# Kernel optimization log

Hardware: AMD Instinct MI355X
Metric: run time of the kernel (lower is better)

Reference implementation:

```python
import jax, jax.numpy as jnp
import numpy as np


def setup_inputs() -> dict:
    key = jax.random.key(0)
    ks = jax.random.split(key, 7)
    B, N, H, BIN = 16, 96, 256, 11
    std = 0.1
    return {
        "inputs": jax.random.normal(ks[0], (B, N, H), dtype=jnp.float32),
        "bin_features": jax.random.normal(ks[1], (B, N, N, BIN), dtype=jnp.float32),
        "W_atom": jax.random.normal(ks[2], (H, H), dtype=jnp.float32) * std,
        "W_bin": jax.random.normal(ks[3], (BIN, H), dtype=jnp.float32) * std,
        "b_bin": jnp.zeros((H,), dtype=jnp.float32),
        "w_score": jax.random.normal(ks[4], (H, 1), dtype=jnp.float32) * std,
        "b_score": jnp.zeros((1,), dtype=jnp.float32),
    }


def reference(inputs, bin_features, W_atom, W_bin, b_bin, w_score, b_score):
    # inputs: [B, N, H]; bin_features: [B, N, N, BIN]
    h1 = inputs[:, None, :, :]            # [B, 1, N, H] (atom_hiddens1)
    h2 = inputs[:, :, None, :]            # [B, N, 1, H] (atom_hiddens2)
    atom_pair = h1 + h2                   # [B, N, N, H]
    # Dense(no bias) on pair + Dense(bias) on bin features, then relu
    att_hidden = jax.nn.relu(
        jnp.einsum("bijh,hk->bijk", atom_pair, W_atom)
        + jnp.einsum("bijc,ck->bijk", bin_features, W_bin)
        + b_bin
    )                                      # [B, N, N, H]
    att_score = jax.nn.sigmoid(jnp.einsum("bijk,ko->bijo", att_hidden, w_score) + b_score)  # [B, N, N, 1]
    # att_context = score * atom_hiddens1 (broadcast over i), summed over j (axis 2)
    context = jnp.einsum("bijo,bjh->bih", att_score, inputs)  # [B, N, H]
    return context, atom_pair
```

## Files before the change

kernel.cpp:

```cpp
#include <hip/hip_runtime.h>
#include <math.h>

#define BB 16
#define NN 96
#define HH 256
#define NBIN 11
#define NBPAD 12

template <int CTRL>
__device__ __forceinline__ float dpp_add(float x) {
    int t = __builtin_amdgcn_update_dpp(0, __float_as_int(x),
                                        CTRL, 0xf, 0xf, true);
    return x + __int_as_float(t);
}

__device__ __forceinline__ float wave64_sum_uniform(float x) {
    x = dpp_add<0x111>(x);
    x = dpp_add<0x112>(x);
    x = dpp_add<0x114>(x);
    x = dpp_add<0x118>(x);
    x = dpp_add<0x142>(x);
    x = dpp_add<0x143>(x);
    return __int_as_float(__builtin_amdgcn_readlane(__float_as_int(x), 63));
}

#define ROWS_PER_BLOCK 4

__global__ __launch_bounds__(HH) void proj_kernel(
    const float* __restrict__ inputs,
    const float* __restrict__ W_atom,
    const float* __restrict__ b_bin,
    float* __restrict__ proj)
{
    __shared__ float rows[ROWS_PER_BLOCK][HH];
    const int r0 = blockIdx.x * ROWS_PER_BLOCK;
    const int k  = threadIdx.x;

    #pragma unroll
    for (int r = 0; r < ROWS_PER_BLOCK; ++r)
        rows[r][k] = inputs[(size_t)(r0 + r) * HH + k];
    __syncthreads();

    float acc[ROWS_PER_BLOCK];
    #pragma unroll
    for (int r = 0; r < ROWS_PER_BLOCK; ++r) acc[r] = 0.f;

    #pragma unroll 8
    for (int h = 0; h < HH; ++h) {
        const float w = W_atom[(size_t)h * HH + k];
        #pragma unroll
        for (int r = 0; r < ROWS_PER_BLOCK; ++r)
            acc[r] = fmaf(rows[r][h], w, acc[r]);
    }

    const float halfb = 0.5f * b_bin[k];
    #pragma unroll
    for (int r = 0; r < ROWS_PER_BLOCK; ++r)
        proj[(size_t)(r0 + r) * HH + k] = acc[r] + halfb;
}

__global__ __launch_bounds__(256) void pair_ctx_kernel(
    const float* __restrict__ inputs,
    const float* __restrict__ bin_features,
    const float* __restrict__ W_bin,
    const float* __restrict__ w_score,
    const float* __restrict__ b_score,
    const float* __restrict__ proj,
    float* __restrict__ atom_pair,
    float* __restrict__ context)
{
    const int bi   = blockIdx.x;
    const int b    = bi / NN;
    const int lane = threadIdx.x & 63;
    const int wave = threadIdx.x >> 6;
    const int k4   = lane << 2;

    __shared__ float binf[NN * NBPAD];
    __shared__ float partial[3][HH];

    {
        const float* bp = bin_features + (size_t)bi * NN * NBIN;
        for (int t = threadIdx.x; t < NN * NBIN; t += 256)
            binf[(t / NBIN) * NBPAD + (t % NBIN)] = bp[t];
    }

    const float4 in_i = *(const float4*)(inputs + (size_t)bi * HH + k4);
    const float4 pr_i = *(const float4*)(proj   + (size_t)bi * HH + k4);
    const float4 ws   = *(const float4*)(w_score + k4);
    const float  bsc  = b_score[0];

    float4 wb[NBIN];
    #pragma unroll
    for (int c = 0; c < NBIN; ++c)
        wb[c] = *(const float4*)(W_bin + c * HH + k4);

    const float* inb = inputs + (size_t)b * NN * HH + k4;
    const float* prb = proj   + (size_t)b * NN * HH + k4;
    float*       apb = atom_pair + (size_t)bi * NN * HH + k4;

    __syncthreads();

    float4 acc = make_float4(0.f, 0.f, 0.f, 0.f);

    for (int t = 0; t < 6; ++t) {
        const int j0 = wave + 16 * t;

        float4 inj[4], prj[4];
        #pragma unroll
        for (int u = 0; u < 4; ++u) {
            inj[u] = *(const float4*)(inb + (size_t)(j0 + 4 * u) * HH);
            prj[u] = *(const float4*)(prb + (size_t)(j0 + 4 * u) * HH);
        }

        #pragma unroll
        for (int u = 0; u < 4; ++u) {
            float4 ap;
            ap.x = in_i.x + inj[u].x;  ap.y = in_i.y + inj[u].y;
            ap.z = in_i.z + inj[u].z;  ap.w = in_i.w + inj[u].w;
            *(float4*)(apb + (size_t)(j0 + 4 * u) * HH) = ap;
        }

        float part[4];
        #pragma unroll
        for (int u = 0; u < 4; ++u) {
            const float4* bf4 = (const float4*)&binf[(j0 + 4 * u) * NBPAD];
            const float4 bq0 = bf4[0];
            const float4 bq1 = bf4[1];
            const float4 bq2 = bf4[2];
            const float bc[NBIN] = { bq0.x, bq0.y, bq0.z, bq0.w,
                                     bq1.x, bq1.y, bq1.z, bq1.w,
                                     bq2.x, bq2.y, bq2.z };

            float4 v;
            v.x = pr_i.x + prj[u].x;  v.y = pr_i.y + prj[u].y;
            v.z = pr_i.z + prj[u].z;  v.w = pr_i.w + prj[u].w;
            #pragma unroll
            for (int c = 0; c < NBIN; ++c) {
                v.x = fmaf(bc[c], wb[c].x, v.x);
                v.y = fmaf(bc[c], wb[c].y, v.y);
                v.z = fmaf(bc[c], wb[c].z, v.z);
                v.w = fmaf(bc[c], wb[c].w, v.w);
            }
            v.x = fmaxf(v.x, 0.f); v.y = fmaxf(v.y, 0.f);
            v.z = fmaxf(v.z, 0.f); v.w = fmaxf(v.w, 0.f);
            part[u] = v.x * ws.x + v.y * ws.y + v.z * ws.z + v.w * ws.w;
        }

        float s[4];
        #pragma unroll
        for (int u = 0; u < 4; ++u) {
            const float tot = wave64_sum_uniform(part[u]);
            s[u] = 1.f / (1.f + __expf(-(tot + bsc)));
        }

        #pragma unroll
        for (int u = 0; u < 4; ++u) {
            acc.x = fmaf(s[u], inj[u].x, acc.x);
            acc.y = fmaf(s[u], inj[u].y, acc.y);
            acc.z = fmaf(s[u], inj[u].z, acc.z);
            acc.w = fmaf(s[u], inj[u].w, acc.w);
        }
    }

    if (wave > 0) *(float4*)(&partial[wave - 1][k4]) = acc;
    __syncthreads();
    if (wave == 0) {
        #pragma unroll
        for (int w = 0; w < 3; ++w) {
            const float4 pw = *(const float4*)(&partial[w][k4]);
            acc.x += pw.x; acc.y += pw.y; acc.z += pw.z; acc.w += pw.w;
        }
        *(float4*)(context + (size_t)bi * HH + k4) = acc;
    }
}

extern "C" void kernel_launch(void* const* d_in, const int* in_sizes, int n_in,
                              void* d_out, int out_size, void* d_ws, size_t ws_size,
                              hipStream_t stream)
{
    const float* inputs       = (const float*)d_in[0];
    const float* bin_features = (const float*)d_in[1];
    const float* W_atom       = (const float*)d_in[2];
    const float* W_bin        = (const float*)d_in[3];
    const float* b_bin        = (const float*)d_in[4];
    const float* w_score      = (const float*)d_in[5];
    const float* b_score      = (const float*)d_in[6];

    float* context   = (float*)d_out;
    float* atom_pair = (float*)d_out + (size_t)BB * NN * HH;

    float* proj = (float*)d_ws;

    proj_kernel<<<(BB * NN) / ROWS_PER_BLOCK, HH, 0, stream>>>(
        inputs, W_atom, b_bin, proj);

    pair_ctx_kernel<<<BB * NN, 256, 0, stream>>>(
        inputs, bin_features, W_bin, w_score, b_score, proj,
        atom_pair, context);
}
```

Measured before the change: 51.72 us.

## Warp-specialize pair kernel: two waves store atom_pair, two compute scores

Splits the four waves of each block by role. Waves 2-3 only read inputs rows and stream the large atom_pair output, while waves 0-1 do the bin-feature projection, ReLU, score reduction and context accumulation over all 96 j. The aim is to overlap the store-bound atom_pair traffic with the compute-bound score path and to shrink the shared-memory partial reduction. The risk is that the compute waves now each handle twice as many j values, so the critical path may lengthen. The two roles also rely on matching __syncthreads counts across divergent branches.

```diff
diff --git a/kernel.cpp b/kernel.cpp
--- a/kernel.cpp
+++ b/kernel.cpp
@@ -76,7 +76,7 @@
     const int k4   = lane << 2;
 
     __shared__ float binf[NN * NBPAD];
-    __shared__ float partial[3][HH];
+    __shared__ float partial[HH];
 
     {
         const float* bp = bin_features + (size_t)bi * NN * NBIN;
@@ -84,93 +84,106 @@
             binf[(t / NBIN) * NBPAD + (t % NBIN)] = bp[t];
     }
 
-    const float4 in_i = *(const float4*)(inputs + (size_t)bi * HH + k4);
-    const float4 pr_i = *(const float4*)(proj   + (size_t)bi * HH + k4);
-    const float4 ws   = *(const float4*)(w_score + k4);
-    const float  bsc  = b_score[0];
-
-    float4 wb[NBIN];
-    #pragma unroll
-    for (int c = 0; c < NBIN; ++c)
-        wb[c] = *(const float4*)(W_bin + c * HH + k4);
-
     const float* inb = inputs + (size_t)b * NN * HH + k4;
-    const float* prb = proj   + (size_t)b * NN * HH + k4;
-    float*       apb = atom_pair + (size_t)bi * NN * HH + k4;
-
-    __syncthreads();
-
-    float4 acc = make_float4(0.f, 0.f, 0.f, 0.f);
-
-    for (int t = 0; t < 6; ++t) {
-        const int j0 = wave + 16 * t;
-
-        float4 inj[4], prj[4];
+
+    if (wave >= 2) {
+        const float4 in_i = *(const float4*)(inputs + (size_t)bi * HH + k4);
+        float* apb = atom_pair + (size_t)bi * NN * HH + k4;
+        const int ww = wave - 2;
+
+        __syncthreads();
+
+        for (int t = 0; t < 12; ++t) {
+            const int j0 = 8 * t + 4 * ww;
+            float4 r[4];
+            #pragma unroll
+            for (int u = 0; u < 4; ++u)
+                r[u] = *(const float4*)(inb + (size_t)(j0 + u) * HH);
+            #pragma unroll
+            for (int u = 0; u < 4; ++u) {
+                float4 ap;
+                ap.x = in_i.x + r[u].x;  ap.y = in_i.y + r[u].y;
+                ap.z = in_i.z + r[u].z;  ap.w = in_i.w + r[u].w;
+                *(float4*)(apb + (size_t)(j0 + u) * HH) = ap;
+            }
+        }
+
+        __syncthreads();
+    } else {
+        const float4 pr_i = *(const float4*)(proj + (size_t)bi * HH + k4);
+        const float4 ws   = *(const float4*)(w_score + k4);
+        const float  bsc  = b_score[0];
+
+        float4 wb[NBIN];
         #pragma unroll
-        for (int u = 0; u < 4; ++u) {
-            inj[u] = *(const float4*)(inb + (size_t)(j0 + 4 * u) * HH);
-            prj[u] = *(const float4*)(prb + (size_t)(j0 + 4 * u) * HH);
+        for (int c = 0; c < NBIN; ++c)
+            wb[c] = *(const float4*)(W_bin + c * HH + k4);
+
+        const float* prb = proj + (size_t)b * NN * HH + k4;
+
+        __syncthreads();
+
+        float4 acc = make_float4(0.f, 0.f, 0.f, 0.f);
+
+        for (int t = 0; t < 12; ++t) {
+            const int j0 = 8 * t + 4 * wave;
+
+            float4 inj[4], prj[4];
+            #pragma unroll
+            for (int u = 0; u < 4; ++u) {
+                inj[u] = *(const float4*)(inb + (size_t)(j0 + u) * HH);
+                prj[u] = *(const float4*)(prb + (size_t)(j0 + u) * HH);
+            }
+
+            float part[4];
+            #pragma unroll
+            for (int u = 0; u < 4; ++u) {
+                const float4* bf4 = (const float4*)&binf[(j0 + u) * NBPAD];
+                const float4 bq0 = bf4[0];
+                const float4 bq1 = bf4[1];
+                const float4 bq2 = bf4[2];
+                const float bc[NBIN] = { bq0.x, bq0.y, bq0.z, bq0.w,
+                                         bq1.x, bq1.y, bq1.z, bq1.w,
+                                         bq2.x, bq2.y, bq2.z };
+
+                float4 v;
+                v.x = pr_i.x + prj[u].x;  v.y = pr_i.y + prj[u].y;
+                v.z = pr_i.z + prj[u].z;  v.w = pr_i.w + prj[u].w;
+                #pragma unroll
+                for (int c = 0; c < NBIN; ++c) {
+                    v.x = fmaf(bc[c], wb[c].x, v.x);
+                    v.y = fmaf(bc[c], wb[c].y, v.y);
+                    v.z = fmaf(bc[c], wb[c].z, v.z);
+                    v.w = fmaf(bc[c], wb[c].w, v.w);
+                }
+                v.x = fmaxf(v.x, 0.f); v.y = fmaxf(v.y, 0.f);
+                v.z = fmaxf(v.z, 0.f); v.w = fmaxf(v.w, 0.f);
+                part[u] = v.x * ws.x + v.y * ws.y + v.z * ws.z + v.w * ws.w;
+            }
+
+            float s[4];
+            #pragma unroll
+            for (int u = 0; u < 4; ++u) {
+                const float tot = wave64_sum_uniform(part[u]);
+                s[u] = 1.f / (1.f + __expf(-(tot + bsc)));
+            }
+
+            #pragma unroll
+            for (int u = 0; u < 4; ++u) {
+                acc.x = fmaf(s[u], inj[u].x, acc.x);
+                acc.y = fmaf(s[u], inj[u].y, acc.y);
+                acc.z = fmaf(s[u], inj[u].z, acc.z);
+                acc.w = fmaf(s[u], inj[u].w, acc.w);
+            }
         }
 
-        #pragma unroll
-        for (int u = 0; u < 4; ++u) {
-            float4 ap;
-            ap.x = in_i.x + inj[u].x;  ap.y = in_i.y + inj[u].y;
-            ap.z = in_i.z + inj[u].z;  ap.w = in_i.w + inj[u].w;
-            *(float4*)(apb + (size_t)(j0 + 4 * u) * HH) = ap;
+        if (wave == 1) *(float4*)(&partial[k4]) = acc;
+        __syncthreads();
+        if (wave == 0) {
+            const float4 pw = *(const float4*)(&partial[k4]);
+            acc.x += pw.x; acc.y += pw.y; acc.z += pw.z; acc.w += pw.w;
+            *(float4*)(context + (size_t)bi * HH + k4) = acc;
         }
-
-        float part[4];
-        #pragma unroll
-        for (int u = 0; u < 4; ++u) {
-            const float4* bf4 = (const float4*)&binf[(j0 + 4 * u) * NBPAD];
-            const float4 bq0 = bf4[0];
-            const float4 bq1 = bf4[1];
-            const float4 bq2 = bf4[2];
-            const float bc[NBIN] = { bq0.x, bq0.y, bq0.z, bq0.w,
-                                     bq1.x, bq1.y, bq1.z, bq1.w,
-                                     bq2.x, bq2.y, bq2.z };
-
-            float4 v;
-            v.x = pr_i.x + prj[u].x;  v.y = pr_i.y + prj[u].y;
-            v.z = pr_i.z + prj[u].z;  v.w = pr_i.w + prj[u].w;
-            #pragma unroll
-            for (int c = 0; c < NBIN; ++c) {
-                v.x = fmaf(bc[c], wb[c].x, v.x);
-                v.y = fmaf(bc[c], wb[c].y, v.y);
-                v.z = fmaf(bc[c], wb[c].z, v.z);
-                v.w = fmaf(bc[c], wb[c].w, v.w);
-            }
-            v.x = fmaxf(v.x, 0.f); v.y = fmaxf(v.y, 0.f);
-            v.z = fmaxf(v.z, 0.f); v.w = fmaxf(v.w, 0.f);
-            part[u] = v.x * ws.x + v.y * ws.y + v.z * ws.z + v.w * ws.w;
-        }
-
-        float s[4];
-        #pragma unroll
-        for (int u = 0; u < 4; ++u) {
-            const float tot = wave64_sum_uniform(part[u]);
-            s[u] = 1.f / (1.f + __expf(-(tot + bsc)));
-        }
-
-        #pragma unroll
-        for (int u = 0; u < 4; ++u) {
-            acc.x = fmaf(s[u], inj[u].x, acc.x);
-            acc.y = fmaf(s[u], inj[u].y, acc.y);
-            acc.z = fmaf(s[u], inj[u].z, acc.z);
-            acc.w = fmaf(s[u], inj[u].w, acc.w);
-        }
-    }
-
-    if (wave > 0) *(float4*)(&partial[wave - 1][k4]) = acc;
-    __syncthreads();
-    if (wave == 0) {
-        #pragma unroll
-        for (int w = 0; w < 3; ++w) {
-            const float4 pw = *(const float4*)(&partial[w][k4]);
-            acc.x += pw.x; acc.y += pw.y; acc.z += pw.z; acc.w += pw.w;
-        }
-        *(float4*)(context + (size_t)bi * HH + k4) = acc;
     }
 }
 
```

New measurement: 65.12 us. +25.9%, slower.

## Process two query rows per block to reuse j-row loads across i

Applied to the files above, without the earlier changes.

The pair/context kernel now handles two consecutive i rows per block, so each loaded inputs[j] and proj[j] float4 serves both rows. This halves the global reads of j-side data and halves the grid size. Launch bounds now request 4 blocks per CU, and the projection kernel uses 3 rows per block, giving more blocks there. The risks are higher register pressure from the two accumulators and fewer blocks to spread across the CUs.

```diff
diff --git a/kernel.cpp b/kernel.cpp
--- a/kernel.cpp
+++ b/kernel.cpp
@@ -6,6 +6,7 @@
 #define HH 256
 #define NBIN 11
 #define NBPAD 12
+#define IB 2
 
 template <int CTRL>
 __device__ __forceinline__ float dpp_add(float x) {
@@ -24,7 +25,7 @@
     return __int_as_float(__builtin_amdgcn_readlane(__float_as_int(x), 63));
 }
 
-#define ROWS_PER_BLOCK 4
+#define ROWS_PER_BLOCK 3
 
 __global__ __launch_bounds__(HH) void proj_kernel(
     const float* __restrict__ inputs,
@@ -59,7 +60,7 @@
         proj[(size_t)(r0 + r) * HH + k] = acc[r] + halfb;
 }
 
-__global__ __launch_bounds__(256) void pair_ctx_kernel(
+__global__ __launch_bounds__(256, 4) void pair_ctx_kernel(
     const float* __restrict__ inputs,
     const float* __restrict__ bin_features,
     const float* __restrict__ W_bin,
@@ -69,108 +70,134 @@
     float* __restrict__ atom_pair,
     float* __restrict__ context)
 {
-    const int bi   = blockIdx.x;
-    const int b    = bi / NN;
+    const int blk  = blockIdx.x;
+    const int b    = blk / (NN / IB);
+    const int ip   = blk % (NN / IB);
+    const int bi0  = b * NN + IB * ip;
     const int lane = threadIdx.x & 63;
     const int wave = threadIdx.x >> 6;
     const int k4   = lane << 2;
 
-    __shared__ float binf[NN * NBPAD];
-    __shared__ float partial[3][HH];
+    __shared__ float binf[IB * NN * NBPAD];
+    __shared__ float partial[3][IB * HH];
 
     {
-        const float* bp = bin_features + (size_t)bi * NN * NBIN;
-        for (int t = threadIdx.x; t < NN * NBIN; t += 256)
+        const float* bp = bin_features + (size_t)bi0 * NN * NBIN;
+        for (int t = threadIdx.x; t < IB * NN * NBIN; t += 256)
             binf[(t / NBIN) * NBPAD + (t % NBIN)] = bp[t];
     }
 
-    const float4 in_i = *(const float4*)(inputs + (size_t)bi * HH + k4);
-    const float4 pr_i = *(const float4*)(proj   + (size_t)bi * HH + k4);
-    const float4 ws   = *(const float4*)(w_score + k4);
-    const float  bsc  = b_score[0];
+    const float4 in_i0 = *(const float4*)(inputs + (size_t)bi0 * HH + k4);
+    const float4 in_i1 = *(const float4*)(inputs + (size_t)(bi0 + 1) * HH + k4);
+    const float4 pr_i0 = *(const float4*)(proj   + (size_t)bi0 * HH + k4);
+    const float4 pr_i1 = *(const float4*)(proj   + (size_t)(bi0 + 1) * HH + k4);
+    const float4 ws    = *(const float4*)(w_score + k4);
+    const float  bsc   = b_score[0];
 
     float4 wb[NBIN];
     #pragma unroll
     for (int c = 0; c < NBIN; ++c)
         wb[c] = *(const float4*)(W_bin + c * HH + k4);
 
-    const float* inb = inputs + (size_t)b * NN * HH + k4;
-    const float* prb = proj   + (size_t)b * NN * HH + k4;
-    float*       apb = atom_pair + (size_t)bi * NN * HH + k4;
+    const float* inb  = inputs + (size_t)b * NN * HH + k4;
+    const float* prb  = proj   + (size_t)b * NN * HH + k4;
+    float*       apb0 = atom_pair + (size_t)bi0 * NN * HH + k4;
+    float*       apb1 = atom_pair + (size_t)(bi0 + 1) * NN * HH + k4;
 
     __syncthreads();
 
-    float4 acc = make_float4(0.f, 0.f, 0.f, 0.f);
-
-    for (int t = 0; t < 6; ++t) {
-        const int j0 = wave + 16 * t;
-
-        float4 inj[4], prj[4];
-        #pragma unroll
-        for (int u = 0; u < 4; ++u) {
+    float4 acc0 = make_float4(0.f, 0.f, 0.f, 0.f);
+    float4 acc1 = make_float4(0.f, 0.f, 0.f, 0.f);
+
+    for (int t = 0; t < 12; ++t) {
+        const int j0 = wave + 8 * t;
+
+        float4 inj[2], prj[2];
+        #pragma unroll
+        for (int u = 0; u < 2; ++u) {
             inj[u] = *(const float4*)(inb + (size_t)(j0 + 4 * u) * HH);
             prj[u] = *(const float4*)(prb + (size_t)(j0 + 4 * u) * HH);
         }
 
         #pragma unroll
-        for (int u = 0; u < 4; ++u) {
+        for (int u = 0; u < 2; ++u) {
             float4 ap;
-            ap.x = in_i.x + inj[u].x;  ap.y = in_i.y + inj[u].y;
-            ap.z = in_i.z + inj[u].z;  ap.w = in_i.w + inj[u].w;
-            *(float4*)(apb + (size_t)(j0 + 4 * u) * HH) = ap;
+            ap.x = in_i0.x + inj[u].x;  ap.y = in_i0.y + inj[u].y;
+            ap.z = in_i0.z + inj[u].z;  ap.w = in_i0.w + inj[u].w;
+            *(float4*)(apb0 + (size_t)(j0 + 4 * u) * HH) = ap;
+            ap.x = in_i1.x + inj[u].x;  ap.y = in_i1.y + inj[u].y;
+            ap.z = in_i1.z + inj[u].z;  ap.w = in_i1.w + inj[u].w;
+            *(float4*)(apb1 + (size_t)(j0 + 4 * u) * HH) = ap;
         }
 
         float part[4];
         #pragma unroll
-        for (int u = 0; u < 4; ++u) {
-            const float4* bf4 = (const float4*)&binf[(j0 + 4 * u) * NBPAD];
-            const float4 bq0 = bf4[0];
-            const float4 bq1 = bf4[1];
-            const float4 bq2 = bf4[2];
-            const float bc[NBIN] = { bq0.x, bq0.y, bq0.z, bq0.w,
-                                     bq1.x, bq1.y, bq1.z, bq1.w,
-                                     bq2.x, bq2.y, bq2.z };
-
-            float4 v;
-            v.x = pr_i.x + prj[u].x;  v.y = pr_i.y + prj[u].y;
-            v.z = pr_i.z + prj[u].z;  v.w = pr_i.w + prj[u].w;
+        for (int u = 0; u < 2; ++u) {
+            const int j = j0 + 4 * u;
             #pragma unroll
-            for (int c = 0; c < NBIN; ++c) {
-                v.x = fmaf(bc[c], wb[c].x, v.x);
-                v.y = fmaf(bc[c], wb[c].y, v.y);
-                v.z = fmaf(bc[c], wb[c].z, v.z);
-                v.w = fmaf(bc[c], wb[c].w, v.w);
+            for (int ii = 0; ii < 2; ++ii) {
+                const float4* bf4 =
+                    (const float4*)&binf[(ii * NN + j) * NBPAD];
+                const float4 bq0 = bf4[0];
+                const float4 bq1 = bf4[1];
+                const float4 bq2 = bf4[2];
+                const float bc[NBIN] = { bq0.x, bq0.y, bq0.z, bq0.w,
+                                         bq1.x, bq1.y, bq1.z, bq1.w,
+                                         bq2.x, bq2.y, bq2.z };
+
+                const float4 pri = ii ? pr_i1 : pr_i0;
+                float4 v;
+                v.x = pri.x + prj[u].x;  v.y = pri.y + prj[u].y;
+                v.z = pri.z + prj[u].z;  v.w = pri.w + prj[u].w;
+                #pragma unroll
+                for (int c = 0; c < NBIN; ++c) {
+                    v.x = fmaf(bc[c], wb[c].x, v.x);
+                    v.y = fmaf(bc[c], wb[c].y, v.y);
+                    v.z = fmaf(bc[c], wb[c].z, v.z);
+                    v.w = fmaf(bc[c], wb[c].w, v.w);
+                }
+                v.x = fmaxf(v.x, 0.f); v.y = fmaxf(v.y, 0.f);
+                v.z = fmaxf(v.z, 0.f); v.w = fmaxf(v.w, 0.f);
+                part[2 * u + ii] =
+                    v.x * ws.x + v.y * ws.y + v.z * ws.z + v.w * ws.w;
             }
-            v.x = fmaxf(v.x, 0.f); v.y = fmaxf(v.y, 0.f);
-            v.z = fmaxf(v.z, 0.f); v.w = fmaxf(v.w, 0.f);
-            part[u] = v.x * ws.x + v.y * ws.y + v.z * ws.z + v.w * ws.w;
         }
 
         float s[4];
         #pragma unroll
-        for (int u = 0; u < 4; ++u) {
-            const float tot = wave64_sum_uniform(part[u]);
-            s[u] = 1.f / (1.f + __expf(-(tot + bsc)));
-        }
-
-        #pragma unroll
-        for (int u = 0; u < 4; ++u) {
-            acc.x = fmaf(s[u], inj[u].x, acc.x);
-            acc.y = fmaf(s[u], inj[u].y, acc.y);
-            acc.z = fmaf(s[u], inj[u].z, acc.z);
-            acc.w = fmaf(s[u], inj[u].w, acc.w);
-        }
-    }
-
-    if (wave > 0) *(float4*)(&partial[wave - 1][k4]) = acc;
+        for (int p = 0; p < 4; ++p) {
+            const float tot = wave64_sum_uniform(part[p]);
+            s[p] = 1.f / (1.f + __expf(-(tot + bsc)));
+        }
+
+        #pragma unroll
+        for (int u = 0; u < 2; ++u) {
+            acc0.x = fmaf(s[2 * u],     inj[u].x, acc0.x);
+            acc0.y = fmaf(s[2 * u],     inj[u].y, acc0.y);
+            acc0.z = fmaf(s[2 * u],     inj[u].z, acc0.z);
+            acc0.w = fmaf(s[2 * u],     inj[u].w, acc0.w);
+            acc1.x = fmaf(s[2 * u + 1], inj[u].x, acc1.x);
+            acc1.y = fmaf(s[2 * u + 1], inj[u].y, acc1.y);
+            acc1.z = fmaf(s[2 * u + 1], inj[u].z, acc1.z);
+            acc1.w = fmaf(s[2 * u + 1], inj[u].w, acc1.w);
+        }
+    }
+
+    if (wave > 0) {
+        *(float4*)(&partial[wave - 1][k4]) = acc0;
+        *(float4*)(&partial[wave - 1][HH + k4]) = acc1;
+    }
     __syncthreads();
     if (wave == 0) {
         #pragma unroll
         for (int w = 0; w < 3; ++w) {
-            const float4 pw = *(const float4*)(&partial[w][k4]);
-            acc.x += pw.x; acc.y += pw.y; acc.z += pw.z; acc.w += pw.w;
-        }
-        *(float4*)(context + (size_t)bi * HH + k4) = acc;
+            const float4 p0 = *(const float4*)(&partial[w][k4]);
+            const float4 p1 = *(const float4*)(&partial[w][HH + k4]);
+            acc0.x += p0.x; acc0.y += p0.y; acc0.z += p0.z; acc0.w += p0.w;
+            acc1.x += p1.x; acc1.y += p1.y; acc1.z += p1.z; acc1.w += p1.w;
+        }
+        *(float4*)(context + (size_t)bi0 * HH + k4) = acc0;
+        *(float4*)(context + (size_t)(bi0 + 1) * HH + k4) = acc1;
     }
 }
 
@@ -194,7 +221,7 @@
     proj_kernel<<<(BB * NN) / ROWS_PER_BLOCK, HH, 0, stream>>>(
         inputs, W_atom, b_bin, proj);
 
-    pair_ctx_kernel<<<BB * NN, 256, 0, stream>>>(
+    pair_ctx_kernel<<<(BB * NN) / IB, 256, 0, stream>>>(
         inputs, bin_features, W_bin, w_score, b_score, proj,
         atom_pair, context);
 }
```

Result: faster. 50.37 us (-2.6%).
